# Performance work log

Measured on AMD Instinct MI355X. Metric: run time of the kernel, lower is better.

Reference implementation:

```python
import jax, jax.numpy as jnp
import numpy as np

EPS = 1e-12  # matches torch F.normalize default eps
TEMPERATURE = 0.07

def _l2_normalize(x):
    norm = jnp.sqrt(jnp.sum(x * x, axis=-1, keepdims=True))
    return x / jnp.maximum(norm, EPS)

def setup_inputs() -> dict:
    key = jax.random.key(0)
    k1, k2 = jax.random.split(key)
    N, D = 4096, 1024
    z1 = jax.random.normal(k1, (N, D), dtype=jnp.float32)
    z2 = jax.random.normal(k2, (N, D), dtype=jnp.float32)
    return {"z1": z1, "z2": z2}

def reference(z1, z2):
    # L2-normalize both sets; cosine similarity of unit vectors is a dot product,
    # so the broadcast CosineSimilarity collapses to a single GEMM.
    z1n = _l2_normalize(z1)
    z2n = _l2_normalize(z2)
    logits = jnp.einsum('nd,md->nm', z1n, z2n) / TEMPERATURE  # [N, N]
    # CrossEntropyLoss with labels = arange(N): mean of -log_softmax diagonal.
    logp = jax.nn.log_softmax(logits, axis=-1)
    loss = -jnp.mean(jnp.diagonal(logp))
    return loss
```

## Files before the change

kernel.cpp:

```cpp
#include <hip/hip_runtime.h>

#define N_ROWS 4096
#define DIM 1024
#define INV_T (1.0f / 0.07f)
#define FP8_SCALE 16.0f
#define EXP_SCALE (INV_T * 1.44269504088896f / 256.0f)
#define BK 128
#define NJT 32

typedef __attribute__((ext_vector_type(4))) float floatx4;
typedef __attribute__((ext_vector_type(4))) int int4x;
typedef __attribute__((ext_vector_type(8))) int int8x;

#if __has_builtin(__builtin_amdgcn_cvt_pk_fp8_f32)
__device__ inline unsigned int pack4_e4m3(float x, float y, float z, float w) {
    int p = __builtin_amdgcn_cvt_pk_fp8_f32(x, y, 0, false);
    p = __builtin_amdgcn_cvt_pk_fp8_f32(z, w, p, true);
    return (unsigned int)p;
}
#else
__device__ inline unsigned int f2e4m3(float x) {
    unsigned int u = __float_as_uint(x);
    unsigned int s = (u >> 24) & 0x80u;
    int e = (int)((u >> 23) & 0xffu);
    unsigned int m = u & 0x7fffffu;
    if (e < 121) return s;
    unsigned int t = m >> 20;
    unsigned int rest = m & 0xFFFFFu;
    t += (rest > 0x80000u) || (rest == 0x80000u && (t & 1u));
    int e8 = e - 120;
    if (t == 8u) { t = 0u; e8 += 1; }
    return s | ((unsigned int)e8 << 3) | t;
}
__device__ inline unsigned int pack4_e4m3(float x, float y, float z, float w) {
    return f2e4m3(x) | (f2e4m3(y) << 8) | (f2e4m3(z) << 16) | (f2e4m3(w) << 24);
}
#endif

__global__ __launch_bounds__(256) void k_normalize(
    const float* __restrict__ z1, const float* __restrict__ z2,
    unsigned char* __restrict__ z1f, unsigned char* __restrict__ z2f,
    float* __restrict__ diag, float* __restrict__ out) {
    const int lane = threadIdx.x & 63, wave = threadIdx.x >> 6;
    const int row = blockIdx.x * 4 + wave;

    if (blockIdx.x == 0 && threadIdx.x == 0) out[0] = 0.f;

    const float4* A = reinterpret_cast<const float4*>(z1 + (size_t)row * DIM);
    const float4* B = reinterpret_cast<const float4*>(z2 + (size_t)row * DIM);
    float4 a[4], b[4];
    #pragma unroll
    for (int rep = 0; rep < 4; ++rep) {
        a[rep] = A[lane + 64 * rep];
        b[rep] = B[lane + 64 * rep];
    }

    float s11 = 0.f, s22 = 0.f, s12 = 0.f;
    #pragma unroll
    for (int rep = 0; rep < 4; ++rep) {
        s11 += a[rep].x * a[rep].x + a[rep].y * a[rep].y
             + a[rep].z * a[rep].z + a[rep].w * a[rep].w;
        s22 += b[rep].x * b[rep].x + b[rep].y * b[rep].y
             + b[rep].z * b[rep].z + b[rep].w * b[rep].w;
        s12 += a[rep].x * b[rep].x + a[rep].y * b[rep].y
             + a[rep].z * b[rep].z + a[rep].w * b[rep].w;
    }
    #pragma unroll
    for (int m = 32; m >= 1; m >>= 1) {
        s11 += __shfl_xor(s11, m, 64);
        s22 += __shfl_xor(s22, m, 64);
        s12 += __shfl_xor(s12, m, 64);
    }

    const float n1 = fmaxf(sqrtf(s11), 1e-12f);
    const float n2 = fmaxf(sqrtf(s22), 1e-12f);
    if (lane == 0) diag[row] = s12 / (n1 * n2) * INV_T;
    const float i1 = FP8_SCALE / n1, i2 = FP8_SCALE / n2;

    unsigned int* O1 = reinterpret_cast<unsigned int*>(z1f + (size_t)row * DIM);
    unsigned int* O2 = reinterpret_cast<unsigned int*>(z2f + (size_t)row * DIM);
    #pragma unroll
    for (int rep = 0; rep < 4; ++rep) {
        O1[lane + 64 * rep] = pack4_e4m3(a[rep].x * i1, a[rep].y * i1,
                                         a[rep].z * i1, a[rep].w * i1);
        O2[lane + 64 * rep] = pack4_e4m3(b[rep].x * i2, b[rep].y * i2,
                                         b[rep].z * i2, b[rep].w * i2);
    }
}

__global__ __launch_bounds__(256) void k_gemm_sumexp(
    const unsigned char* __restrict__ z1f, const unsigned char* __restrict__ z2f,
    float* __restrict__ P) {
    __shared__ __attribute__((aligned(16))) unsigned char As[2][128 * BK];
    __shared__ __attribute__((aligned(16))) unsigned char Bs[2][128 * BK];

    const int iT = blockIdx.y, jT = blockIdx.x;
    const int lane = threadIdx.x & 63, wave = threadIdx.x >> 6;
    const int wm = wave >> 1, wn = wave & 1;
    const int ml = lane & 15, q = lane >> 4;
    const int i0 = iT * 128, j0 = jT * 128;

    const int srow = lane >> 3;
    const int sg = ((lane & 7) ^ srow) * 16;

    const int rs = ml & 7;
    const int slotL = ((2 * q) ^ rs) * 16;
    const int slotH = ((2 * q + 1) ^ rs) * 16;

    floatx4 acc[4][4];
    #pragma unroll
    for (int mt = 0; mt < 4; ++mt)
        #pragma unroll
        for (int nt = 0; nt < 4; ++nt)
            acc[mt][nt] = (floatx4){0.f, 0.f, 0.f, 0.f};

    auto stage = [&](int tile, int db) {
        const int k0 = tile * BK;
        #pragma unroll
        for (int c = 0; c < 4; ++c) {
            const int issue = wave * 4 + c;
            const int row = issue * 8 + srow;
            const unsigned char* gA = z1f + (size_t)(i0 + row) * DIM + k0 + sg;
            const unsigned char* gB = z2f + (size_t)(j0 + row) * DIM + k0 + sg;
            __builtin_amdgcn_global_load_lds(
                (const __attribute__((address_space(1))) void*)gA,
                (__attribute__((address_space(3))) void*)(&As[db][issue * 1024]),
                16, 0, 0);
            __builtin_amdgcn_global_load_lds(
                (const __attribute__((address_space(1))) void*)gB,
                (__attribute__((address_space(3))) void*)(&Bs[db][issue * 1024]),
                16, 0, 0);
        }
    };

    int8x af[2][4], bf[2][4];
    auto ldfrags = [&](int sl, int db) {
        #pragma unroll
        for (int t = 0; t < 4; ++t) {
            const unsigned char* rowA = &As[db][0] + (wm * 64 + t * 16 + ml) * BK;
            const unsigned char* rowB = &Bs[db][0] + (wn * 64 + t * 16 + ml) * BK;
            int4x aL = *reinterpret_cast<const int4x*>(rowA + slotL);
            int4x aH = *reinterpret_cast<const int4x*>(rowA + slotH);
            int4x bLo = *reinterpret_cast<const int4x*>(rowB + slotL);
            int4x bHi = *reinterpret_cast<const int4x*>(rowB + slotH);
            af[sl][t] = __builtin_shufflevector(aL, aH, 0, 1, 2, 3, 4, 5, 6, 7);
            bf[sl][t] = __builtin_shufflevector(bLo, bHi, 0, 1, 2, 3, 4, 5, 6, 7);
        }
    };

    stage(0, 0);
    asm volatile("s_waitcnt vmcnt(0)" ::: "memory");
    __builtin_amdgcn_s_barrier();
    ldfrags(0, 0);
    stage(1, 1);

    #pragma unroll
    for (int kt = 0; kt < 8; ++kt) {
        const int cur = kt & 1;
        asm volatile("s_waitcnt vmcnt(0) lgkmcnt(0)" ::: "memory");
        __builtin_amdgcn_s_barrier();
        if (kt < 7) ldfrags(cur ^ 1, cur ^ 1);
        if (kt < 6) stage(kt + 2, cur);
        #pragma unroll
        for (int mt = 0; mt < 4; ++mt)
            #pragma unroll
            for (int nt = 0; nt < 4; ++nt)
                acc[mt][nt] = __builtin_amdgcn_mfma_scale_f32_16x16x128_f8f6f4(
                    af[cur][mt], bf[cur][nt], acc[mt][nt],
                    0 , 0 ,
                    0, 0x7F , 0, 0x7F );
    }

    float vv[4][4];
    #pragma unroll
    for (int mt = 0; mt < 4; ++mt) {
        #pragma unroll
        for (int r = 0; r < 4; ++r) {
            float v = 0.f;
            #pragma unroll
            for (int nt = 0; nt < 4; ++nt)
                v += __builtin_amdgcn_exp2f(acc[mt][nt][r] * EXP_SCALE);
            v += __shfl_xor(v, 1, 64);
            v += __shfl_xor(v, 2, 64);
            v += __shfl_xor(v, 4, 64);
            v += __shfl_xor(v, 8, 64);
            vv[mt][r] = v;
        }
    }
    float* Pl = reinterpret_cast<float*>(&As[0][0]);
    if (wn == 1 && ml == 0) {
        #pragma unroll
        for (int mt = 0; mt < 4; ++mt)
            #pragma unroll
            for (int r = 0; r < 4; ++r)
                Pl[wm * 64 + mt * 16 + q * 4 + r] = vv[mt][r];
    }
    __syncthreads();
    if (wn == 0 && ml == 0) {
        #pragma unroll
        for (int mt = 0; mt < 4; ++mt)
            #pragma unroll
            for (int r = 0; r < 4; ++r) {
                const int ri = wm * 64 + mt * 16 + q * 4 + r;
                P[jT * N_ROWS + i0 + ri] = vv[mt][r] + Pl[ri];
            }
    }
}

__global__ __launch_bounds__(128) void k_finalize(
    const float* __restrict__ P, const float* __restrict__ diag,
    float* __restrict__ out) {
    const int t = threadIdx.x;
    const int i = blockIdx.x * 128 + t;
    float s = 0.f;
    #pragma unroll
    for (int jt = 0; jt < NJT; ++jt)
        s += P[jt * N_ROWS + i];
    float v = logf(s) - diag[i];
    #pragma unroll
    for (int m = 32; m >= 1; m >>= 1)
        v += __shfl_xor(v, m, 64);
    __shared__ float r[2];
    if ((t & 63) == 0) r[t >> 6] = v;
    __syncthreads();
    if (t == 0) atomicAdd(out, (r[0] + r[1]) * (1.0f / N_ROWS));
}

extern "C" void kernel_launch(void* const* d_in, const int* in_sizes, int n_in,
                              void* d_out, int out_size, void* d_ws, size_t ws_size,
                              hipStream_t stream) {
    const float* z1 = (const float*)d_in[0];
    const float* z2 = (const float*)d_in[1];

    char* ws = (char*)d_ws;
    unsigned char* z1f = (unsigned char*)ws;
    unsigned char* z2f = (unsigned char*)(ws + (size_t)N_ROWS * DIM);
    float* diag = (float*)(ws + (size_t)N_ROWS * DIM * 2);
    float* P = diag + N_ROWS;

    k_normalize<<<N_ROWS / 4, 256, 0, stream>>>(z1, z2, z1f, z2f, diag,
                                                (float*)d_out);
    k_gemm_sumexp<<<dim3(NJT, 32), 256, 0, stream>>>(z1f, z2f, P);
    k_finalize<<<32, 128, 0, stream>>>(P, diag, (float*)d_out);
}
```

Measured before the change: 101.4 us.

## Load A operand directly from global into registers, staging only B through LDS

The GEMM kernel stops staging the z1 (A) tile through shared memory. Each wave now reads its A fragments straight from global memory into double-buffered registers, one k-tile ahead. Only B still goes through the LDS double buffer, with explicit vmcnt waits and barriers reworked to match. This halves LDS footprint and LDS read/write traffic, but the two waves sharing each A row block now load it twice from global/L2. It also raises register pressure and relies on hand-counted vmcnt values being correct.

```diff
diff --git a/kernel.cpp b/kernel.cpp
--- a/kernel.cpp
+++ b/kernel.cpp
@@ -91,7 +91,6 @@
 __global__ __launch_bounds__(256) void k_gemm_sumexp(
     const unsigned char* __restrict__ z1f, const unsigned char* __restrict__ z2f,
     float* __restrict__ P) {
-    __shared__ __attribute__((aligned(16))) unsigned char As[2][128 * BK];
     __shared__ __attribute__((aligned(16))) unsigned char Bs[2][128 * BK];
 
     const int iT = blockIdx.y, jT = blockIdx.x;
@@ -107,6 +106,8 @@
     const int slotL = ((2 * q) ^ rs) * 16;
     const int slotH = ((2 * q + 1) ^ rs) * 16;
 
+    const unsigned char* aBase = z1f + (size_t)(i0 + wm * 64 + ml) * DIM + q * 32;
+
     floatx4 acc[4][4];
     #pragma unroll
     for (int mt = 0; mt < 4; ++mt)
@@ -114,18 +115,13 @@
         for (int nt = 0; nt < 4; ++nt)
             acc[mt][nt] = (floatx4){0.f, 0.f, 0.f, 0.f};
 
-    auto stage = [&](int tile, int db) {
+    auto stageB = [&](int tile, int db) {
         const int k0 = tile * BK;
         #pragma unroll
         for (int c = 0; c < 4; ++c) {
             const int issue = wave * 4 + c;
             const int row = issue * 8 + srow;
-            const unsigned char* gA = z1f + (size_t)(i0 + row) * DIM + k0 + sg;
             const unsigned char* gB = z2f + (size_t)(j0 + row) * DIM + k0 + sg;
-            __builtin_amdgcn_global_load_lds(
-                (const __attribute__((address_space(1))) void*)gA,
-                (__attribute__((address_space(3))) void*)(&As[db][issue * 1024]),
-                16, 0, 0);
             __builtin_amdgcn_global_load_lds(
                 (const __attribute__((address_space(1))) void*)gB,
                 (__attribute__((address_space(3))) void*)(&Bs[db][issue * 1024]),
@@ -133,42 +129,50 @@
         }
     };
 
-    int8x af[2][4], bf[2][4];
-    auto ldfrags = [&](int sl, int db) {
+    int8x af[2][4];
+    auto loadA = [&](int sl, int tile) {
+        const int k0 = tile * BK;
         #pragma unroll
         for (int t = 0; t < 4; ++t) {
-            const unsigned char* rowA = &As[db][0] + (wm * 64 + t * 16 + ml) * BK;
-            const unsigned char* rowB = &Bs[db][0] + (wn * 64 + t * 16 + ml) * BK;
-            int4x aL = *reinterpret_cast<const int4x*>(rowA + slotL);
-            int4x aH = *reinterpret_cast<const int4x*>(rowA + slotH);
+            const unsigned char* p = aBase + (size_t)(t * 16) * DIM + k0;
+            int4x lo = *reinterpret_cast<const int4x*>(p);
+            int4x hi = *reinterpret_cast<const int4x*>(p + 16);
+            af[sl][t] = __builtin_shufflevector(lo, hi, 0, 1, 2, 3, 4, 5, 6, 7);
+        }
+    };
+
+    stageB(0, 0);
+    loadA(0, 0);
+    stageB(1, 1);
+    asm volatile("s_waitcnt vmcnt(12)" ::: "memory");
+    __builtin_amdgcn_s_barrier();
+
+    #pragma unroll
+    for (int kt = 0; kt < 8; ++kt) {
+        const int cur = kt & 1;
+        int8x bf[4];
+        #pragma unroll
+        for (int t = 0; t < 4; ++t) {
+            const unsigned char* rowB = &Bs[cur][0] + (wn * 64 + t * 16 + ml) * BK;
             int4x bLo = *reinterpret_cast<const int4x*>(rowB + slotL);
             int4x bHi = *reinterpret_cast<const int4x*>(rowB + slotH);
-            af[sl][t] = __builtin_shufflevector(aL, aH, 0, 1, 2, 3, 4, 5, 6, 7);
-            bf[sl][t] = __builtin_shufflevector(bLo, bHi, 0, 1, 2, 3, 4, 5, 6, 7);
-        }
-    };
-
-    stage(0, 0);
-    asm volatile("s_waitcnt vmcnt(0)" ::: "memory");
-    __builtin_amdgcn_s_barrier();
-    ldfrags(0, 0);
-    stage(1, 1);
-
-    #pragma unroll
-    for (int kt = 0; kt < 8; ++kt) {
-        const int cur = kt & 1;
-        asm volatile("s_waitcnt vmcnt(0) lgkmcnt(0)" ::: "memory");
+            bf[t] = __builtin_shufflevector(bLo, bHi, 0, 1, 2, 3, 4, 5, 6, 7);
+        }
+        if (kt < 7) loadA(cur ^ 1, kt + 1);
+        asm volatile("s_waitcnt lgkmcnt(0)" ::: "memory");
         __builtin_amdgcn_s_barrier();
-        if (kt < 7) ldfrags(cur ^ 1, cur ^ 1);
-        if (kt < 6) stage(kt + 2, cur);
+        if (kt < 6) stageB(kt + 2, cur);
         #pragma unroll
         for (int mt = 0; mt < 4; ++mt)
             #pragma unroll
             for (int nt = 0; nt < 4; ++nt)
                 acc[mt][nt] = __builtin_amdgcn_mfma_scale_f32_16x16x128_f8f6f4(
-                    af[cur][mt], bf[cur][nt], acc[mt][nt],
+                    af[cur][mt], bf[nt], acc[mt][nt],
                     0 , 0 ,
                     0, 0x7F , 0, 0x7F );
+        if (kt < 6)      { asm volatile("s_waitcnt vmcnt(12)" ::: "memory"); }
+        else if (kt < 7) { asm volatile("s_waitcnt vmcnt(8)" ::: "memory"); }
+        __builtin_amdgcn_s_barrier();
     }
 
     float vv[4][4];
@@ -187,7 +191,7 @@
             vv[mt][r] = v;
         }
     }
-    float* Pl = reinterpret_cast<float*>(&As[0][0]);
+    float* Pl = reinterpret_cast<float*>(&Bs[0][0]);
     if (wn == 1 && ml == 0) {
         #pragma unroll
         for (int mt = 0; mt < 4; ++mt)
```

Result: slower. 115.7 us (+14.2%).
